# Optimization experiments

Hardware: AMD Instinct MI355X
Metric: run time of the kernel (lower is better)

The kernel has to match this reference:

```python
import math
import jax, jax.numpy as jnp
import numpy as np

B, T, C, H = 4, 2048, 1024, 16
HD = C // H

def gelu_tanh(x):
    return 0.5 * x * (1.0 + jnp.tanh(jnp.sqrt(2.0 / jnp.pi) * (x + 0.044715 * x * x * x)))

def layernorm(x, w, b, eps=1e-5):
    mu = jnp.mean(x, axis=-1, keepdims=True)
    var = jnp.var(x, axis=-1, keepdims=True)
    return (x - mu) * jax.lax.rsqrt(var + eps) * w + b

def setup_inputs() -> dict:
    key = jax.random.key(0)
    ks = jax.random.split(key, 8)
    s = 0.02
    return {
        "x": jax.random.normal(ks[0], (B, T, C), dtype=jnp.float32),
        "ln1_w": jnp.ones((C,), jnp.float32), "ln1_b": jnp.zeros((C,), jnp.float32),
        "attn_w": jax.random.normal(ks[1], (C, 3 * C), jnp.float32) * s,
        "attn_b": jnp.zeros((3 * C,), jnp.float32),
        "proj_w": jax.random.normal(ks[2], (C, C), jnp.float32) * s,
        "proj_b": jnp.zeros((C,), jnp.float32),
        "ln2_w": jnp.ones((C,), jnp.float32), "ln2_b": jnp.zeros((C,), jnp.float32),
        "fc_w": jax.random.normal(ks[3], (C, 4 * C), jnp.float32) * s,
        "fc_b": jnp.zeros((4 * C,), jnp.float32),
        "fc_proj_w": jax.random.normal(ks[4], (4 * C, C), jnp.float32) * s,
        "fc_proj_b": jnp.zeros((C,), jnp.float32),
    }

def block(x, ln1_w, ln1_b, attn_w, attn_b, proj_w, proj_b,
          ln2_w, ln2_b, fc_w, fc_b, fc_proj_w, fc_proj_b):
    # --- causal self-attention ---
    h = layernorm(x, ln1_w, ln1_b)
    qkv = h @ attn_w + attn_b                      # [B,T,3C]
    q, k, v = jnp.split(qkv, 3, axis=-1)
    q = q.reshape(B, T, H, HD).transpose(0, 2, 1, 3)  # [B,H,T,hd]
    k = k.reshape(B, T, H, HD).transpose(0, 2, 1, 3)
    v = v.reshape(B, T, H, HD).transpose(0, 2, 1, 3)
    att = jnp.einsum('bhqd,bhkd->bhqk', q, k) * (1.0 / math.sqrt(HD))
    mask = jnp.tril(jnp.ones((T, T), dtype=bool))
    att = jnp.where(mask, att, -jnp.inf)
    att = jax.nn.softmax(att, axis=-1)
    y = jnp.einsum('bhqk,bhkd->bhqd', att, v)
    y = y.transpose(0, 2, 1, 3).reshape(B, T, C)
    x = x + (y @ proj_w + proj_b)
    # --- MLP ---
    h = layernorm(x, ln2_w, ln2_b)
    h = gelu_tanh(h @ fc_w + fc_b)
    x = x + (h @ fc_proj_w + fc_proj_b)
    return x

def reference(x, ln1_w, ln1_b, attn_w, attn_b, proj_w, proj_b,
              ln2_w, ln2_b, fc_w, fc_b, fc_proj_w, fc_proj_b):
    return block(x, ln1_w, ln1_b, attn_w, attn_b, proj_w, proj_b,
                 ln2_w, ln2_b, fc_w, fc_b, fc_proj_w, fc_proj_b)
```

## Files before the change

kernel.cpp:

```cpp
#include <hip/hip_runtime.h>
#include <stdint.h>

#define TSEQ 2048
#define CDIM 1024
#define NHEAD 16
#define HDIM 64
#define NROWS 8192

typedef __bf16 bf16x8 __attribute__((ext_vector_type(8)));
typedef float f32x4 __attribute__((ext_vector_type(4)));
typedef float f32x16 __attribute__((ext_vector_type(16)));

__device__ __forceinline__ unsigned short f2bf(float f) {
  unsigned u = __builtin_bit_cast(unsigned, f);
  u = u + 0x7fffu + ((u >> 16) & 1u);
  return (unsigned short)(u >> 16);
}

__device__ __forceinline__ unsigned cvt_pk_bf16(float a, float b) {
  unsigned r;
  asm("v_cvt_pk_bf16_f32 %0, %1, %2" : "=v"(r) : "v"(a), "v"(b));
  return r;
}

__device__ __forceinline__ float gelu_f(float x) {
  float x3 = x * x * x;
  float z = 0.7978845608028654f * (x + 0.044715f * x3);
  float e = __expf(2.f * z);
  float t = 1.f - 2.f / (e + 1.f);
  return 0.5f * x * (1.f + t);
}

__device__ __forceinline__ void ldg_lds16(void* lds, const void* gsrc) {
  __builtin_amdgcn_global_load_lds(
      (__attribute__((address_space(1))) unsigned int*)(uintptr_t)gsrc,
      (__attribute__((address_space(3))) unsigned int*)lds,
      16, 0, 0);
}

__global__ __launch_bounds__(256) void k_wtrans(const float* __restrict__ W,
                                                unsigned short* __restrict__ Wt,
                                                int K, int N) {
  __shared__ unsigned short tl[32][40];
  int n0 = blockIdx.x * 32, k0 = blockIdx.y * 32;
  int tid = threadIdx.x;
  int r = tid >> 3, c4 = (tid & 7) * 4;
  float4 v = *(const float4*)(W + (size_t)(k0 + r) * N + n0 + c4);
  ushort4 o;
  o.x = f2bf(v.x); o.y = f2bf(v.y); o.z = f2bf(v.z); o.w = f2bf(v.w);
  *(ushort4*)&tl[r][c4] = o;
  __syncthreads();
  int n = tid >> 3, k4 = (tid & 7) * 4;
  ushort4 w;
  w.x = tl[k4 + 0][n]; w.y = tl[k4 + 1][n]; w.z = tl[k4 + 2][n]; w.w = tl[k4 + 3][n];
  *(ushort4*)(Wt + (size_t)(n0 + n) * K + k0 + k4) = w;
}

__global__ __launch_bounds__(256) void k_ln(const float* __restrict__ x,
                                            const float* __restrict__ w,
                                            const float* __restrict__ b,
                                            unsigned short* __restrict__ out) {
  int row = blockIdx.x;
  int tid = threadIdx.x;
  const float* xr = x + (size_t)row * CDIM;
  float4 v = *(const float4*)(xr + tid * 4);
  float s = v.x + v.y + v.z + v.w;
  float s2 = v.x * v.x + v.y * v.y + v.z * v.z + v.w * v.w;
#pragma unroll
  for (int off = 32; off; off >>= 1) {
    s += __shfl_xor(s, off);
    s2 += __shfl_xor(s2, off);
  }
  __shared__ float rbuf[8];
  int wv = tid >> 6, lane = tid & 63;
  if (lane == 0) { rbuf[wv] = s; rbuf[4 + wv] = s2; }
  __syncthreads();
  float S1 = rbuf[0] + rbuf[1] + rbuf[2] + rbuf[3];
  float S2 = rbuf[4] + rbuf[5] + rbuf[6] + rbuf[7];
  float mean = S1 * (1.f / CDIM);
  float var = S2 * (1.f / CDIM) - mean * mean;
  float rstd = rsqrtf(var + 1e-5f);
  float4 wv4 = *(const float4*)(w + tid * 4);
  float4 bv4 = *(const float4*)(b + tid * 4);
  ushort4 o;
  o.x = f2bf((v.x - mean) * rstd * wv4.x + bv4.x);
  o.y = f2bf((v.y - mean) * rstd * wv4.y + bv4.y);
  o.z = f2bf((v.z - mean) * rstd * wv4.z + bv4.z);
  o.w = f2bf((v.w - mean) * rstd * wv4.w + bv4.w);
  *(ushort4*)(out + (size_t)row * CDIM + tid * 4) = o;
}

template <int EPI>
__global__ __launch_bounds__(512, 2)
void k_gemm8(const unsigned short* __restrict__ A,
             const unsigned short* __restrict__ Bt,
             const float* __restrict__ bias,
             const float* __restrict__ resid,
             void* __restrict__ Cout,
             int M, int N, int K) {
  __shared__ __align__(16) unsigned short lds[3 * 24576];
  const int tid = threadIdx.x;
  const int wid = tid >> 6, lane = tid & 63;
  const int wm = wid >> 2, wn = wid & 3;
  const int fr = lane & 15, fq = lane >> 4;

  const int gx = gridDim.x;
  int flat = blockIdx.y * gx + blockIdx.x;
  {
    const int nwg = gx * gridDim.y;
    int q = nwg >> 3, r = nwg & 7;
    int xcd = flat & 7, idx = flat >> 3;
    flat = (xcd < r ? xcd * (q + 1) : r * (q + 1) + (xcd - r) * q) + idx;
  }
  const int bx = flat % gx, by = flat / gx;
  const long brow = (long)by * 128, bcol = (long)bx * 256;

  const int lrow = lane >> 3;
  const int kby = ((lane & 7) << 4) ^ (((lane >> 5) & 1) << 5);
  const char* gA = (const char*)(A + ((size_t)(brow + wid * 16 + lrow)) * K) + kby;
  const char* gB = (const char*)(Bt + ((size_t)(bcol + wid * 32 + lrow)) * K) + kby;

  const int NT = K >> 6;

#define STAGE_A(i, t, bf_)                                              \
  ldg_lds16((char*)(lds + (bf_) * 24576) + (wid * 2 + (i)) * 1024,      \
            gA + ((size_t)(i) * 8 * K + (size_t)(t) * 64) * 2)
#define STAGE_B(j, t, bf_)                                              \
  ldg_lds16((char*)(lds + (bf_) * 24576 + 8192) + (wid * 4 + (j)) * 1024, \
            gB + ((size_t)(j) * 8 * K + (size_t)(t) * 64) * 2)

  STAGE_A(0, 0, 0); STAGE_A(1, 0, 0);
  STAGE_B(0, 0, 0); STAGE_B(1, 0, 0); STAGE_B(2, 0, 0); STAGE_B(3, 0, 0);
  STAGE_A(0, 1, 1); STAGE_A(1, 1, 1);
  STAGE_B(0, 1, 1); STAGE_B(1, 1, 1); STAGE_B(2, 1, 1); STAGE_B(3, 1, 1);

  f32x4 acc[4][4];
  const f32x4 vzero = {0.f, 0.f, 0.f, 0.f};
#pragma unroll
  for (int m = 0; m < 4; ++m)
#pragma unroll
    for (int n = 0; n < 4; ++n) acc[m][n] = vzero;

  const int swz = (fq << 4) ^ ((fr & 4) << 3);
  int buf = 0;
  for (int t = 0; t < NT; ++t) {
    if (t + 1 < NT) asm volatile("s_waitcnt vmcnt(6)" ::: "memory");
    else            asm volatile("s_waitcnt vmcnt(0)" ::: "memory");
    __builtin_amdgcn_s_barrier();
    __builtin_amdgcn_sched_barrier(0);
    const char* pA = (const char*)(lds + buf * 24576);
    const char* pB = pA + 16384;
    int nbuf = buf + 2; if (nbuf >= 3) nbuf -= 3;
    if (t + 2 < NT) { STAGE_A(0, t + 2, nbuf); STAGE_A(1, t + 2, nbuf); STAGE_B(0, t + 2, nbuf); }
    bf16x8 bfrag[4][2];
#pragma unroll
    for (int n = 0; n < 4; ++n)
#pragma unroll
      for (int kh = 0; kh < 2; ++kh)
        bfrag[n][kh] = *(const bf16x8*)(pB + (wn * 64 + n * 16 + fr) * 128 + kh * 64 + swz);
    bf16x8 af01[2][2];
#pragma unroll
    for (int m = 0; m < 2; ++m)
#pragma unroll
      for (int kh = 0; kh < 2; ++kh)
        af01[m][kh] = *(const bf16x8*)(pA + (wm * 64 + m * 16 + fr) * 128 + kh * 64 + swz);
    __builtin_amdgcn_s_setprio(1);
#pragma unroll
    for (int m = 0; m < 2; ++m)
#pragma unroll
      for (int n = 0; n < 4; ++n)
#pragma unroll
        for (int kh = 0; kh < 2; ++kh)
          acc[m][n] = __builtin_amdgcn_mfma_f32_16x16x32_bf16(af01[m][kh], bfrag[n][kh], acc[m][n], 0, 0, 0);
    __builtin_amdgcn_s_setprio(0);
    __builtin_amdgcn_s_barrier();
    if (t + 2 < NT) { STAGE_B(1, t + 2, nbuf); STAGE_B(2, t + 2, nbuf); STAGE_B(3, t + 2, nbuf); }
    bf16x8 af23[2][2];
#pragma unroll
    for (int m = 0; m < 2; ++m)
#pragma unroll
      for (int kh = 0; kh < 2; ++kh)
        af23[m][kh] = *(const bf16x8*)(pA + (wm * 64 + (m + 2) * 16 + fr) * 128 + kh * 64 + swz);
    __builtin_amdgcn_s_setprio(1);
#pragma unroll
    for (int m = 0; m < 2; ++m)
#pragma unroll
      for (int n = 0; n < 4; ++n)
#pragma unroll
        for (int kh = 0; kh < 2; ++kh)
          acc[m + 2][n] = __builtin_amdgcn_mfma_f32_16x16x32_bf16(af23[m][kh], bfrag[n][kh], acc[m + 2][n], 0, 0, 0);
    __builtin_amdgcn_s_setprio(0);
    buf = buf + 1; if (buf == 3) buf = 0;
  }
#undef STAGE_A
#undef STAGE_B

#pragma unroll
  for (int m = 0; m < 4; ++m) {
    long row = brow + wm * 64 + m * 16 + fq * 4;
#pragma unroll
    for (int n = 0; n < 4; ++n) {
      long col = bcol + wn * 64 + n * 16 + fr;
      float bv = bias[col];
#pragma unroll
      for (int r = 0; r < 4; ++r) {
        float v = acc[m][n][r] + bv;
        long idx = (row + r) * (long)N + col;
        if (EPI == 0) {
          ((unsigned short*)Cout)[idx] = f2bf(v);
        } else if (EPI == 1) {
          ((unsigned short*)Cout)[idx] = f2bf(gelu_f(v));
        } else {
          ((float*)Cout)[idx] = v + resid[idx];
        }
      }
    }
  }
}

__global__ __launch_bounds__(256) void k_build_vt(const unsigned short* __restrict__ qkv,
                                                  unsigned short* __restrict__ vt) {
  __shared__ __align__(16) unsigned short tl[64][80];
  int bh = blockIdx.x, b = bh >> 4, h = bh & 15;
  int t0 = blockIdx.y * 64;
  int tid = threadIdx.x;
  int r = tid >> 2, cb = (tid & 3) * 16;
  const unsigned short* src =
      qkv + (size_t)(b * TSEQ + t0 + r) * (3 * CDIM) + 2 * CDIM + h * HDIM + cb;
  *(uint4*)&tl[r][cb] = *(const uint4*)src;
  *(uint4*)&tl[r][cb + 8] = *(const uint4*)(src + 8);
  __syncthreads();
  int d = tid >> 2, tb = (tid & 3) * 16;
  union { unsigned short u[16]; uint4 v[2]; } o;
#pragma unroll
  for (int j = 0; j < 16; ++j) o.u[j] = tl[tb + j][d];
  unsigned short* dst = vt + ((size_t)bh * HDIM + d) * TSEQ + t0 + tb;
  *(uint4*)dst = o.v[0];
  *(uint4*)(dst + 8) = o.v[1];
}

struct QSt {
  f32x16 OTlo, OThi;
  float m, l;
};

__device__ __forceinline__ void attn_qk_sm_pv(
    const bf16x8& k0, const bf16x8& k1, const bf16x8& k2, const bf16x8& k3,
    const bf16x8& v0, const bf16x8& v1, const bf16x8& v2, const bf16x8& v3,
    const bf16x8& q0f, const bf16x8& q1f, const bf16x8& q2f, const bf16x8& q3f,
    QSt& S, bool diag, int lq, int hi) {
  const float SC = 0.125f * 1.44269504088896f;
  f32x16 st;
#pragma unroll
  for (int r = 0; r < 16; ++r) st[r] = 0.f;
  st = __builtin_amdgcn_mfma_f32_32x32x16_bf16(k0, q0f, st, 0, 0, 0);
  st = __builtin_amdgcn_mfma_f32_32x32x16_bf16(k1, q1f, st, 0, 0, 0);
  st = __builtin_amdgcn_mfma_f32_32x32x16_bf16(k2, q2f, st, 0, 0, 0);
  st = __builtin_amdgcn_mfma_f32_32x32x16_bf16(k3, q3f, st, 0, 0, 0);
#pragma unroll
  for (int r = 0; r < 16; ++r) st[r] *= SC;
  if (diag) {
#pragma unroll
    for (int r = 0; r < 16; ++r) {
      int kvl = (r & 3) + 8 * (r >> 2) + 4 * hi;
      if (kvl > lq) st[r] = -1e30f;
    }
  }
  float tmax = st[0];
#pragma unroll
  for (int r = 1; r < 16; ++r) tmax = fmaxf(tmax, st[r]);
  float tm = fmaxf(tmax, __shfl_xor(tmax, 32));
  if (__any(tm > S.m + 8.f)) {
    float mnew = fmaxf(S.m, tm);
    float alpha = __builtin_amdgcn_exp2f(S.m - mnew);
    S.m = mnew;
    S.OTlo *= alpha;
    S.OThi *= alpha;
    S.l *= alpha;
  }
  unsigned c[8];
  float rs = 0.f;
#pragma unroll
  for (int i = 0; i < 8; ++i) {
    float pa = __builtin_amdgcn_exp2f(st[2 * i] - S.m);
    float pb = __builtin_amdgcn_exp2f(st[2 * i + 1] - S.m);
    rs += pa + pb;
    c[i] = cvt_pk_bf16(pa, pb);
  }
  S.l += rs + __shfl_xor(rs, 32);
  unsigned pc[8];
#pragma unroll
  for (int i = 0; i < 8; ++i) pc[i] = __shfl_xor(c[i], 32);
  uint4 w1, w2;
  w1.x = hi ? pc[2] : c[0]; w1.y = hi ? pc[3] : c[1];
  w1.z = hi ? c[2] : pc[0]; w1.w = hi ? c[3] : pc[1];
  w2.x = hi ? pc[6] : c[4]; w2.y = hi ? pc[7] : c[5];
  w2.z = hi ? c[6] : pc[4]; w2.w = hi ? c[7] : pc[5];
  bf16x8 f1 = __builtin_bit_cast(bf16x8, w1);
  bf16x8 f2 = __builtin_bit_cast(bf16x8, w2);
  S.OTlo = __builtin_amdgcn_mfma_f32_32x32x16_bf16(v0, f1, S.OTlo, 0, 0, 0);
  S.OTlo = __builtin_amdgcn_mfma_f32_32x32x16_bf16(v1, f2, S.OTlo, 0, 0, 0);
  S.OThi = __builtin_amdgcn_mfma_f32_32x32x16_bf16(v2, f1, S.OThi, 0, 0, 0);
  S.OThi = __builtin_amdgcn_mfma_f32_32x32x16_bf16(v3, f2, S.OThi, 0, 0, 0);
}

__global__ __launch_bounds__(256, 2) void k_attn(const unsigned short* __restrict__ qkv,
                                                 const unsigned short* __restrict__ vt,
                                                 unsigned short* __restrict__ y) {
  __shared__ __align__(16) unsigned short Ks[2][2048];
  __shared__ __align__(16) unsigned short Vs[2][2048];
  const int bh = blockIdx.x, b = bh >> 4, h = bh & 15;
  const int wv = threadIdx.x >> 6, lane = threadIdx.x & 63;
  const int by = blockIdx.y;
  const int w = by * 4 + wv;
  const int lq = lane & 31, hi = lane >> 5;
  const int ntL = w, ntH = 63 - w;
  const int q0L = w * 32, q0H = (63 - w) * 32;
  const int T = 64 - 4 * by;

  const unsigned short* qrowL = qkv + ((size_t)(b * TSEQ) + q0L + lq) * (3 * CDIM) + h * HDIM;
  const unsigned short* qrowH = qkv + ((size_t)(b * TSEQ) + q0H + lq) * (3 * CDIM) + h * HDIM;
  bf16x8 qL0 = *(const bf16x8*)(qrowL + 0 + hi * 8);
  bf16x8 qL1 = *(const bf16x8*)(qrowL + 16 + hi * 8);
  bf16x8 qL2 = *(const bf16x8*)(qrowL + 32 + hi * 8);
  bf16x8 qL3 = *(const bf16x8*)(qrowL + 48 + hi * 8);
  bf16x8 qH0 = *(const bf16x8*)(qrowH + 0 + hi * 8);
  bf16x8 qH1 = *(const bf16x8*)(qrowH + 16 + hi * 8);
  bf16x8 qH2 = *(const bf16x8*)(qrowH + 32 + hi * 8);
  bf16x8 qH3 = *(const bf16x8*)(qrowH + 48 + hi * 8);

  const int kr = lane & 31, kc = wv * 2 + (lane >> 5);
  const unsigned short* gK =
      qkv + ((size_t)(b * TSEQ) + kr) * (3 * CDIM) + CDIM + h * HDIM + kc * 8;
  const unsigned short* gV = vt + ((size_t)bh * HDIM + lane) * TSEQ + wv * 8;

#define STAGEKV(bf_, tt)                                                  \
  do {                                                                    \
    ldg_lds16((char*)Ks[bf_] + wv * 1024, gK + (size_t)(tt) * 32 * (3 * CDIM)); \
    ldg_lds16((char*)Vs[bf_] + wv * 1024, gV + (tt) * 32);                \
  } while (0)

  QSt SL, SH;
#pragma unroll
  for (int r = 0; r < 16; ++r) {
    SL.OTlo[r] = 0.f; SL.OThi[r] = 0.f; SH.OTlo[r] = 0.f; SH.OThi[r] = 0.f;
  }
  SL.m = -1e30f; SL.l = 0.f; SH.m = -1e30f; SH.l = 0.f;

  STAGEKV(0, 0);
  for (int t = 0; t < T; ++t) {
    __syncthreads();
    if (t + 1 < T) STAGEKV((t + 1) & 1, t + 1);
    if (t <= ntH) {
      const unsigned short* Kb = Ks[t & 1];
      const unsigned short* Vb = Vs[t & 1];
      bf16x8 k0 = *(const bf16x8*)(Kb + (0 + hi) * 256 + lq * 8);
      bf16x8 k1 = *(const bf16x8*)(Kb + (2 + hi) * 256 + lq * 8);
      bf16x8 k2 = *(const bf16x8*)(Kb + (4 + hi) * 256 + lq * 8);
      bf16x8 k3 = *(const bf16x8*)(Kb + (6 + hi) * 256 + lq * 8);
      bf16x8 v0 = *(const bf16x8*)(Vb + hi * 512 + lq * 8);
      bf16x8 v1 = *(const bf16x8*)(Vb + (2 + hi) * 512 + lq * 8);
      bf16x8 v2 = *(const bf16x8*)(Vb + hi * 512 + (lq + 32) * 8);
      bf16x8 v3 = *(const bf16x8*)(Vb + (2 + hi) * 512 + (lq + 32) * 8);
      attn_qk_sm_pv(k0, k1, k2, k3, v0, v1, v2, v3,
                    qH0, qH1, qH2, qH3, SH, t == ntH, lq, hi);
      if (t <= ntL)
        attn_qk_sm_pv(k0, k1, k2, k3, v0, v1, v2, v3,
                      qL0, qL1, qL2, qL3, SL, t == ntL, lq, hi);
    }
  }
#undef STAGEKV

  {
    float inv = 1.f / SH.l;
    unsigned short* yrow = y + ((size_t)(b * TSEQ) + q0H + lq) * CDIM + h * HDIM;
#pragma unroll
    for (int r = 0; r < 16; r += 2) {
      int d = (r & 3) + 8 * (r >> 2) + 4 * hi;
      unsigned lo0 = f2bf(SH.OTlo[r] * inv), lo1 = f2bf(SH.OTlo[r + 1] * inv);
      *(unsigned*)(yrow + d) = lo0 | (lo1 << 16);
      unsigned h0 = f2bf(SH.OThi[r] * inv), h1 = f2bf(SH.OThi[r + 1] * inv);
      *(unsigned*)(yrow + 32 + d) = h0 | (h1 << 16);
    }
  }
  {
    float inv = 1.f / SL.l;
    unsigned short* yrow = y + ((size_t)(b * TSEQ) + q0L + lq) * CDIM + h * HDIM;
#pragma unroll
    for (int r = 0; r < 16; r += 2) {
      int d = (r & 3) + 8 * (r >> 2) + 4 * hi;
      unsigned lo0 = f2bf(SL.OTlo[r] * inv), lo1 = f2bf(SL.OTlo[r + 1] * inv);
      *(unsigned*)(yrow + d) = lo0 | (lo1 << 16);
      unsigned h0 = f2bf(SL.OThi[r] * inv), h1 = f2bf(SL.OThi[r + 1] * inv);
      *(unsigned*)(yrow + 32 + d) = h0 | (h1 << 16);
    }
  }
}

extern "C" void kernel_launch(void* const* d_in, const int* in_sizes, int n_in,
                              void* d_out, int out_size, void* d_ws, size_t ws_size,
                              hipStream_t stream) {
  const float* x = (const float*)d_in[0];
  const float* ln1_w = (const float*)d_in[1];
  const float* ln1_b = (const float*)d_in[2];
  const float* attn_w = (const float*)d_in[3];
  const float* attn_b = (const float*)d_in[4];
  const float* proj_w = (const float*)d_in[5];
  const float* proj_b = (const float*)d_in[6];
  const float* ln2_w = (const float*)d_in[7];
  const float* ln2_b = (const float*)d_in[8];
  const float* fc_w = (const float*)d_in[9];
  const float* fc_b = (const float*)d_in[10];
  const float* fc_proj_w = (const float*)d_in[11];
  const float* fc_proj_b = (const float*)d_in[12];

  char* ws = (char*)d_ws;
  unsigned short* wt_attn = (unsigned short*)(ws + 0);
  unsigned short* wt_proj = (unsigned short*)(ws + 6291456);
  unsigned short* wt_fc = (unsigned short*)(ws + 8388608);
  unsigned short* wt_fcp = (unsigned short*)(ws + 16777216);
  float* x1 = (float*)(ws + 25165824);
  unsigned short* hbuf = (unsigned short*)(ws + 58720256);
  unsigned short* ybuf = (unsigned short*)(ws + 75497472);
  unsigned short* qkvb = (unsigned short*)(ws + 92274688);
  unsigned short* vtb = (unsigned short*)(ws + 142606336);
  unsigned short* gbuf = (unsigned short*)(ws + 92274688);

  k_wtrans<<<dim3(3072 / 32, 1024 / 32), 256, 0, stream>>>(attn_w, wt_attn, 1024, 3072);
  k_wtrans<<<dim3(1024 / 32, 1024 / 32), 256, 0, stream>>>(proj_w, wt_proj, 1024, 1024);
  k_wtrans<<<dim3(4096 / 32, 1024 / 32), 256, 0, stream>>>(fc_w, wt_fc, 1024, 4096);
  k_wtrans<<<dim3(1024 / 32, 4096 / 32), 256, 0, stream>>>(fc_proj_w, wt_fcp, 4096, 1024);

  k_ln<<<NROWS, 256, 0, stream>>>(x, ln1_w, ln1_b, hbuf);

  k_gemm8<0><<<dim3(3072 / 256, NROWS / 128), 512, 0, stream>>>(
      hbuf, wt_attn, attn_b, nullptr, qkvb, NROWS, 3072, 1024);

  k_build_vt<<<dim3(64, TSEQ / 64), 256, 0, stream>>>(qkvb, vtb);

  k_attn<<<dim3(64, 8), 256, 0, stream>>>(qkvb, vtb, ybuf);

  k_gemm8<2><<<dim3(1024 / 256, NROWS / 128), 512, 0, stream>>>(
      ybuf, wt_proj, proj_b, x, x1, NROWS, 1024, 1024);

  k_ln<<<NROWS, 256, 0, stream>>>(x1, ln2_w, ln2_b, hbuf);

  k_gemm8<1><<<dim3(4096 / 256, NROWS / 128), 512, 0, stream>>>(
      hbuf, wt_fc, fc_b, nullptr, gbuf, NROWS, 4096, 1024);

  k_gemm8<2><<<dim3(1024 / 256, NROWS / 128), 512, 0, stream>>>(
      gbuf, wt_fcp, fc_proj_b, x1, (float*)d_out, NROWS, 1024, 4096);
}
```

Baseline: 390.2 us.

## Reshape GEMM tile to 256x128 with 32-wide K steps and new LDS swizzle

The GEMM block tile changes from 128x256 to 256x128 and the K step is halved from 64 to 32. Each warp now covers 128x32 outputs instead of 64x64, and the shared-memory buffers shrink, with a new XOR swizzle for 64-byte rows. Explicit lgkmcnt waits are added before the MFMA groups. The aim is to cut LDS footprint, possibly for better occupancy, but halving K per stage doubles the number of barriers and waits per tile, and the warp shape gives less B-fragment reuse.

New measurement: 379.1 us. -2.9%, faster.

```diff
diff --git a/kernel.cpp b/kernel.cpp
--- a/kernel.cpp
+++ b/kernel.cpp
@@ -98,7 +98,7 @@
              const float* __restrict__ resid,
              void* __restrict__ Cout,
              int M, int N, int K) {
-  __shared__ __align__(16) unsigned short lds[3 * 24576];
+  __shared__ __align__(16) unsigned short lds[3 * 12288];
   const int tid = threadIdx.x;
   const int wid = tid >> 6, lane = tid & 63;
   const int wm = wid >> 2, wn = wid & 3;
@@ -113,82 +113,74 @@
     flat = (xcd < r ? xcd * (q + 1) : r * (q + 1) + (xcd - r) * q) + idx;
   }
   const int bx = flat % gx, by = flat / gx;
-  const long brow = (long)by * 128, bcol = (long)bx * 256;
-
-  const int lrow = lane >> 3;
-  const int kby = ((lane & 7) << 4) ^ (((lane >> 5) & 1) << 5);
-  const char* gA = (const char*)(A + ((size_t)(brow + wid * 16 + lrow)) * K) + kby;
-  const char* gB = (const char*)(Bt + ((size_t)(bcol + wid * 32 + lrow)) * K) + kby;
-
-  const int NT = K >> 6;
-
-#define STAGE_A(i, t, bf_)                                              \
-  ldg_lds16((char*)(lds + (bf_) * 24576) + (wid * 2 + (i)) * 1024,      \
-            gA + ((size_t)(i) * 8 * K + (size_t)(t) * 64) * 2)
-#define STAGE_B(j, t, bf_)                                              \
-  ldg_lds16((char*)(lds + (bf_) * 24576 + 8192) + (wid * 4 + (j)) * 1024, \
-            gB + ((size_t)(j) * 8 * K + (size_t)(t) * 64) * 2)
-
-  STAGE_A(0, 0, 0); STAGE_A(1, 0, 0);
-  STAGE_B(0, 0, 0); STAGE_B(1, 0, 0); STAGE_B(2, 0, 0); STAGE_B(3, 0, 0);
-  STAGE_A(0, 1, 1); STAGE_A(1, 1, 1);
-  STAGE_B(0, 1, 1); STAGE_B(1, 1, 1); STAGE_B(2, 1, 1); STAGE_B(3, 1, 1);
-
-  f32x4 acc[4][4];
+  const long brow = (long)by * 256, bcol = (long)bx * 128;
+
+  const int srow = lane >> 2;
+  const int sby = (((lane & 3) ^ ((lane >> 3) & 3)) << 4);
+  const char* gA = (const char*)(A + ((size_t)(brow + wid * 32 + srow)) * K) + sby;
+  const char* gB = (const char*)(Bt + ((size_t)(bcol + wid * 16 + srow)) * K) + sby;
+
+  const int NT = K >> 5;
+
+#define STAGE_A(i, t, bf_)                                                   \
+  ldg_lds16((char*)lds + (bf_) * 24576 + wid * 2048 + (i) * 1024,            \
+            gA + ((size_t)(i) * 16 * K + (size_t)(t) * 32) * 2)
+#define STAGE_B(t, bf_)                                                      \
+  ldg_lds16((char*)lds + (bf_) * 24576 + 16384 + wid * 1024,                 \
+            gB + ((size_t)(t) * 32) * 2)
+
+  STAGE_A(0, 0, 0); STAGE_A(1, 0, 0); STAGE_B(0, 0);
+  STAGE_A(0, 1, 1); STAGE_A(1, 1, 1); STAGE_B(1, 1);
+
+  f32x4 acc[8][2];
   const f32x4 vzero = {0.f, 0.f, 0.f, 0.f};
 #pragma unroll
-  for (int m = 0; m < 4; ++m)
-#pragma unroll
-    for (int n = 0; n < 4; ++n) acc[m][n] = vzero;
-
-  const int swz = (fq << 4) ^ ((fr & 4) << 3);
+  for (int m = 0; m < 8; ++m) {
+    acc[m][0] = vzero; acc[m][1] = vzero;
+  }
+
+  const int ksw = ((fq ^ ((fr >> 1) & 3)) << 4);
   int buf = 0;
   for (int t = 0; t < NT; ++t) {
-    if (t + 1 < NT) asm volatile("s_waitcnt vmcnt(6)" ::: "memory");
+    if (t + 1 < NT) asm volatile("s_waitcnt vmcnt(3)" ::: "memory");
     else            asm volatile("s_waitcnt vmcnt(0)" ::: "memory");
     __builtin_amdgcn_s_barrier();
     __builtin_amdgcn_sched_barrier(0);
-    const char* pA = (const char*)(lds + buf * 24576);
+    const char* pA = (const char*)lds + buf * 24576;
     const char* pB = pA + 16384;
     int nbuf = buf + 2; if (nbuf >= 3) nbuf -= 3;
-    if (t + 2 < NT) { STAGE_A(0, t + 2, nbuf); STAGE_A(1, t + 2, nbuf); STAGE_B(0, t + 2, nbuf); }
-    bf16x8 bfrag[4][2];
-#pragma unroll
-    for (int n = 0; n < 4; ++n)
-#pragma unroll
-      for (int kh = 0; kh < 2; ++kh)
-        bfrag[n][kh] = *(const bf16x8*)(pB + (wn * 64 + n * 16 + fr) * 128 + kh * 64 + swz);
-    bf16x8 af01[2][2];
-#pragma unroll
-    for (int m = 0; m < 2; ++m)
-#pragma unroll
-      for (int kh = 0; kh < 2; ++kh)
-        af01[m][kh] = *(const bf16x8*)(pA + (wm * 64 + m * 16 + fr) * 128 + kh * 64 + swz);
+    if (t + 2 < NT) { STAGE_A(0, t + 2, nbuf); STAGE_A(1, t + 2, nbuf); }
+    bf16x8 bfrag[2];
+#pragma unroll
+    for (int n = 0; n < 2; ++n)
+      bfrag[n] = *(const bf16x8*)(pB + (wn * 32 + n * 16 + fr) * 64 + ksw);
+    bf16x8 af0[4];
+#pragma unroll
+    for (int m = 0; m < 4; ++m)
+      af0[m] = *(const bf16x8*)(pA + (wm * 128 + m * 16 + fr) * 64 + ksw);
+    asm volatile("s_waitcnt lgkmcnt(0)" ::: "memory");
+    __builtin_amdgcn_sched_barrier(0);
     __builtin_amdgcn_s_setprio(1);
 #pragma unroll
-    for (int m = 0; m < 2; ++m)
-#pragma unroll
-      for (int n = 0; n < 4; ++n)
-#pragma unroll
-        for (int kh = 0; kh < 2; ++kh)
-          acc[m][n] = __builtin_amdgcn_mfma_f32_16x16x32_bf16(af01[m][kh], bfrag[n][kh], acc[m][n], 0, 0, 0);
+    for (int m = 0; m < 4; ++m)
+#pragma unroll
+      for (int n = 0; n < 2; ++n)
+        acc[m][n] = __builtin_amdgcn_mfma_f32_16x16x32_bf16(af0[m], bfrag[n], acc[m][n], 0, 0, 0);
     __builtin_amdgcn_s_setprio(0);
     __builtin_amdgcn_s_barrier();
-    if (t + 2 < NT) { STAGE_B(1, t + 2, nbuf); STAGE_B(2, t + 2, nbuf); STAGE_B(3, t + 2, nbuf); }
-    bf16x8 af23[2][2];
-#pragma unroll
-    for (int m = 0; m < 2; ++m)
-#pragma unroll
-      for (int kh = 0; kh < 2; ++kh)
-        af23[m][kh] = *(const bf16x8*)(pA + (wm * 64 + (m + 2) * 16 + fr) * 128 + kh * 64 + swz);
+    if (t + 2 < NT) STAGE_B(t + 2, nbuf);
+    bf16x8 af1[4];
+#pragma unroll
+    for (int m = 0; m < 4; ++m)
+      af1[m] = *(const bf16x8*)(pA + (wm * 128 + (m + 4) * 16 + fr) * 64 + ksw);
+    asm volatile("s_waitcnt lgkmcnt(0)" ::: "memory");
+    __builtin_amdgcn_sched_barrier(0);
     __builtin_amdgcn_s_setprio(1);
 #pragma unroll
-    for (int m = 0; m < 2; ++m)
-#pragma unroll
-      for (int n = 0; n < 4; ++n)
-#pragma unroll
-        for (int kh = 0; kh < 2; ++kh)
-          acc[m + 2][n] = __builtin_amdgcn_mfma_f32_16x16x32_bf16(af23[m][kh], bfrag[n][kh], acc[m + 2][n], 0, 0, 0);
+    for (int m = 0; m < 4; ++m)
+#pragma unroll
+      for (int n = 0; n < 2; ++n)
+        acc[m + 4][n] = __builtin_amdgcn_mfma_f32_16x16x32_bf16(af1[m], bfrag[n], acc[m + 4][n], 0, 0, 0);
     __builtin_amdgcn_s_setprio(0);
     buf = buf + 1; if (buf == 3) buf = 0;
   }
@@ -196,11 +188,11 @@
 #undef STAGE_B
 
 #pragma unroll
-  for (int m = 0; m < 4; ++m) {
-    long row = brow + wm * 64 + m * 16 + fq * 4;
-#pragma unroll
-    for (int n = 0; n < 4; ++n) {
-      long col = bcol + wn * 64 + n * 16 + fr;
+  for (int m = 0; m < 8; ++m) {
+    long row = brow + wm * 128 + m * 16 + fq * 4;
+#pragma unroll
+    for (int n = 0; n < 2; ++n) {
+      long col = bcol + wn * 32 + n * 16 + fr;
       float bv = bias[col];
 #pragma unroll
       for (int r = 0; r < 4; ++r) {
@@ -433,21 +425,21 @@
 
   k_ln<<<NROWS, 256, 0, stream>>>(x, ln1_w, ln1_b, hbuf);
 
-  k_gemm8<0><<<dim3(3072 / 256, NROWS / 128), 512, 0, stream>>>(
+  k_gemm8<0><<<dim3(3072 / 128, NROWS / 256), 512, 0, stream>>>(
       hbuf, wt_attn, attn_b, nullptr, qkvb, NROWS, 3072, 1024);
 
   k_build_vt<<<dim3(64, TSEQ / 64), 256, 0, stream>>>(qkvb, vtb);
 
   k_attn<<<dim3(64, 8), 256, 0, stream>>>(qkvb, vtb, ybuf);
 
-  k_gemm8<2><<<dim3(1024 / 256, NROWS / 128), 512, 0, stream>>>(
+  k_gemm8<2><<<dim3(1024 / 128, NROWS / 256), 512, 0, stream>>>(
       ybuf, wt_proj, proj_b, x, x1, NROWS, 1024, 1024);
 
   k_ln<<<NROWS, 256, 0, stream>>>(x1, ln2_w, ln2_b, hbuf);
 
-  k_gemm8<1><<<dim3(4096 / 256, NROWS / 128), 512, 0, stream>>>(
+  k_gemm8<1><<<dim3(4096 / 128, NROWS / 256), 512, 0, stream>>>(
       hbuf, wt_fc, fc_b, nullptr, gbuf, NROWS, 4096, 1024);
 
-  k_gemm8<2><<<dim3(1024 / 256, NROWS / 128), 512, 0, stream>>>(
+  k_gemm8<2><<<dim3(1024 / 128, NROWS / 256), 512, 0, stream>>>(
       gbuf, wt_fcp, fc_proj_b, x1, (float*)d_out, NROWS, 1024, 4096);
 }
```

## Halve GEMM K-tile and deepen prefetch to four LDS buffers

Applied to the files above, without the earlier changes.

The bf16 GEMM main loop moves from 64-wide K tiles with a triple buffer to 32-wide K tiles with four LDS buffers, prefetching three stages ahead. Each iteration now needs only one barrier and issues all 16 MFMAs in one block, with a new XOR swizzle for the 64-byte LDS rows. The aim is to hide global-load latency better and cut total LDS use from about 144KB to 96KB. In exchange there are twice as many loop iterations and barriers per K, and less MFMA work between them.

After: 387.8 us. About the same (-0.6%).

```diff
diff --git a/kernel.cpp b/kernel.cpp
--- a/kernel.cpp
+++ b/kernel.cpp
@@ -98,7 +98,7 @@
              const float* __restrict__ resid,
              void* __restrict__ Cout,
              int M, int N, int K) {
-  __shared__ __align__(16) unsigned short lds[3 * 24576];
+  __shared__ __align__(16) unsigned short lds[4 * 12288];
   const int tid = threadIdx.x;
   const int wid = tid >> 6, lane = tid & 63;
   const int wm = wid >> 2, wn = wid & 3;
@@ -115,24 +115,22 @@
   const int bx = flat % gx, by = flat / gx;
   const long brow = (long)by * 128, bcol = (long)bx * 256;
 
-  const int lrow = lane >> 3;
-  const int kby = ((lane & 7) << 4) ^ (((lane >> 5) & 1) << 5);
-  const char* gA = (const char*)(A + ((size_t)(brow + wid * 16 + lrow)) * K) + kby;
-  const char* gB = (const char*)(Bt + ((size_t)(bcol + wid * 32 + lrow)) * K) + kby;
-
-  const int NT = K >> 6;
-
-#define STAGE_A(i, t, bf_)                                              \
-  ldg_lds16((char*)(lds + (bf_) * 24576) + (wid * 2 + (i)) * 1024,      \
-            gA + ((size_t)(i) * 8 * K + (size_t)(t) * 64) * 2)
-#define STAGE_B(j, t, bf_)                                              \
-  ldg_lds16((char*)(lds + (bf_) * 24576 + 8192) + (wid * 4 + (j)) * 1024, \
-            gB + ((size_t)(j) * 8 * K + (size_t)(t) * 64) * 2)
-
-  STAGE_A(0, 0, 0); STAGE_A(1, 0, 0);
-  STAGE_B(0, 0, 0); STAGE_B(1, 0, 0); STAGE_B(2, 0, 0); STAGE_B(3, 0, 0);
-  STAGE_A(0, 1, 1); STAGE_A(1, 1, 1);
-  STAGE_B(0, 1, 1); STAGE_B(1, 1, 1); STAGE_B(2, 1, 1); STAGE_B(3, 1, 1);
+  const int sby = (((lane & 3) ^ ((lane >> 3) & 3)) << 4);
+  const char* gA = (const char*)(A + ((size_t)(brow + wid * 16 + (lane >> 2))) * K) + sby;
+  const char* gB = (const char*)(Bt + ((size_t)(bcol + wid * 32 + (lane >> 2))) * K) + sby;
+
+  const int NT = K >> 5;
+
+#define STAGE_A(t, bf_)                                                 \
+  ldg_lds16((char*)lds + (bf_) * 24576 + wid * 1024,                    \
+            gA + (size_t)(t) * 64)
+#define STAGE_B(i, t, bf_)                                              \
+  ldg_lds16((char*)lds + (bf_) * 24576 + 8192 + (wid * 2 + (i)) * 1024, \
+            gB + (size_t)(i) * 16 * K * 2 + (size_t)(t) * 64)
+
+  STAGE_A(0, 0); STAGE_B(0, 0, 0); STAGE_B(1, 0, 0);
+  STAGE_A(1, 1); STAGE_B(0, 1, 1); STAGE_B(1, 1, 1);
+  STAGE_A(2, 2); STAGE_B(0, 2, 2); STAGE_B(1, 2, 2);
 
   f32x4 acc[4][4];
   const f32x4 vzero = {0.f, 0.f, 0.f, 0.f};
@@ -141,56 +139,33 @@
 #pragma unroll
     for (int n = 0; n < 4; ++n) acc[m][n] = vzero;
 
-  const int swz = (fq << 4) ^ ((fr & 4) << 3);
-  int buf = 0;
+  const int ksw = ((fq ^ ((fr >> 1) & 3)) << 4);
   for (int t = 0; t < NT; ++t) {
-    if (t + 1 < NT) asm volatile("s_waitcnt vmcnt(6)" ::: "memory");
+    if (t + 2 < NT) asm volatile("s_waitcnt vmcnt(6)" ::: "memory");
     else            asm volatile("s_waitcnt vmcnt(0)" ::: "memory");
     __builtin_amdgcn_s_barrier();
     __builtin_amdgcn_sched_barrier(0);
-    const char* pA = (const char*)(lds + buf * 24576);
-    const char* pB = pA + 16384;
-    int nbuf = buf + 2; if (nbuf >= 3) nbuf -= 3;
-    if (t + 2 < NT) { STAGE_A(0, t + 2, nbuf); STAGE_A(1, t + 2, nbuf); STAGE_B(0, t + 2, nbuf); }
-    bf16x8 bfrag[4][2];
+    const int buf = t & 3, nbuf = (t + 3) & 3;
+    if (t + 3 < NT) {
+      STAGE_A(t + 3, nbuf); STAGE_B(0, t + 3, nbuf); STAGE_B(1, t + 3, nbuf);
+    }
+    const char* pA = (const char*)lds + buf * 24576;
+    const char* pB = pA + 8192;
+    bf16x8 af[4], bfr[4];
+#pragma unroll
+    for (int m = 0; m < 4; ++m)
+      af[m] = *(const bf16x8*)(pA + (wm * 64 + m * 16 + fr) * 64 + ksw);
 #pragma unroll
     for (int n = 0; n < 4; ++n)
-#pragma unroll
-      for (int kh = 0; kh < 2; ++kh)
-        bfrag[n][kh] = *(const bf16x8*)(pB + (wn * 64 + n * 16 + fr) * 128 + kh * 64 + swz);
-    bf16x8 af01[2][2];
-#pragma unroll
-    for (int m = 0; m < 2; ++m)
-#pragma unroll
-      for (int kh = 0; kh < 2; ++kh)
-        af01[m][kh] = *(const bf16x8*)(pA + (wm * 64 + m * 16 + fr) * 128 + kh * 64 + swz);
+      bfr[n] = *(const bf16x8*)(pB + (wn * 64 + n * 16 + fr) * 64 + ksw);
     __builtin_amdgcn_s_setprio(1);
 #pragma unroll
-    for (int m = 0; m < 2; ++m)
+    for (int m = 0; m < 4; ++m)
 #pragma unroll
       for (int n = 0; n < 4; ++n)
-#pragma unroll
-        for (int kh = 0; kh < 2; ++kh)
-          acc[m][n] = __builtin_amdgcn_mfma_f32_16x16x32_bf16(af01[m][kh], bfrag[n][kh], acc[m][n], 0, 0, 0);
+        acc[m][n] = __builtin_amdgcn_mfma_f32_16x16x32_bf16(af[m], bfr[n], acc[m][n], 0, 0, 0);
     __builtin_amdgcn_s_setprio(0);
-    __builtin_amdgcn_s_barrier();
-    if (t + 2 < NT) { STAGE_B(1, t + 2, nbuf); STAGE_B(2, t + 2, nbuf); STAGE_B(3, t + 2, nbuf); }
-    bf16x8 af23[2][2];
-#pragma unroll
-    for (int m = 0; m < 2; ++m)
-#pragma unroll
-      for (int kh = 0; kh < 2; ++kh)
-        af23[m][kh] = *(const bf16x8*)(pA + (wm * 64 + (m + 2) * 16 + fr) * 128 + kh * 64 + swz);
-    __builtin_amdgcn_s_setprio(1);
-#pragma unroll
-    for (int m = 0; m < 2; ++m)
-#pragma unroll
-      for (int n = 0; n < 4; ++n)
-#pragma unroll
-        for (int kh = 0; kh < 2; ++kh)
-          acc[m + 2][n] = __builtin_amdgcn_mfma_f32_16x16x32_bf16(af23[m][kh], bfrag[n][kh], acc[m + 2][n], 0, 0, 0);
-    __builtin_amdgcn_s_setprio(0);
-    buf = buf + 1; if (buf == 3) buf = 0;
+    __builtin_amdgcn_sched_barrier(0);
   }
 #undef STAGE_A
 #undef STAGE_B
```
